# Performance work log

Measured on AMD Instinct MI355X. Metric: run time of the kernel, lower is better.

Reference implementation:

```python
import jax, jax.numpy as jnp
import numpy as np

N = 200000          # real (non-pad) faces
P = 8192            # pad entries
PAD = N + P         # padded table size
C_IN = 128
C_OUT = 128


def setup_inputs() -> dict:
    key = jax.random.key(0)
    ks = jax.random.split(key, 6)
    x = jax.random.normal(ks[0], (N, C_IN), jnp.float32)
    # column 0 = the face itself (a real, non-pad index); columns 1..8 = neighbors
    col0 = jnp.arange(N, dtype=jnp.int64)[:, None]
    nbrs = jax.random.randint(ks[1], (N, 8), 0, PAD, dtype=jnp.int64)
    face_neighborhood = jnp.concatenate([col0, nbrs], axis=1)
    face_is_pad = jnp.arange(PAD) >= N  # last P rows are padding
    s = 1.0 / np.sqrt(C_IN).astype(np.float32)
    in_proj_w = jax.random.normal(ks[2], (3 * C_IN, C_IN), jnp.float32) * s
    in_proj_b = jnp.zeros((3 * C_IN,), jnp.float32)
    out_proj_w = jax.random.normal(ks[3], (C_IN, C_IN), jnp.float32) * s
    out_proj_b = jnp.zeros((C_IN,), jnp.float32)
    conv_w = jax.random.normal(ks[4], (C_OUT, C_IN, 1, 2), jnp.float32) * (1.0 / np.sqrt(2.0 * C_IN).astype(np.float32))
    conv_b = jnp.zeros((C_OUT,), jnp.float32)
    return {
        "x": x,
        "face_neighborhood": face_neighborhood,
        "face_is_pad": face_is_pad,
        "pad_size": PAD,
        "in_proj_w": in_proj_w,
        "in_proj_b": in_proj_b,
        "out_proj_w": out_proj_w,
        "out_proj_b": out_proj_b,
        "conv_w": conv_w,
        "conv_b": conv_b,
    }


def reference(x, face_neighborhood, face_is_pad, pad_size,
              in_proj_w, in_proj_b, out_proj_w, out_proj_b, conv_w, conv_b):
    C = x.shape[1]
    H = max(1, C // 32)
    Dh = C // H
    # scatter real features into the padded table (padded_x[~face_is_pad] = x)
    nonpad_idx = jnp.nonzero(~face_is_pad, size=x.shape[0])[0]
    padded_x = jnp.zeros((pad_size, C), x.dtype).at[nonpad_idx].set(x)
    f = padded_x[face_neighborhood]              # [N, 9, C] 9-way gather
    center = f[:, 0]                             # [N, C] query feature
    kv = f[:, 1:]                                # [N, 8, C]
    # torch MultiheadAttention: packed in_proj then per-head scaled dot-product
    q = (center @ in_proj_w[:C].T + in_proj_b[:C]).reshape(-1, 1, H, Dh).transpose(0, 2, 1, 3)       # [N,H,1,Dh]
    k = (kv @ in_proj_w[C:2 * C].T + in_proj_b[C:2 * C]).reshape(-1, 8, H, Dh).transpose(0, 2, 1, 3)  # [N,H,8,Dh]
    v = (kv @ in_proj_w[2 * C:].T + in_proj_b[2 * C:]).reshape(-1, 8, H, Dh).transpose(0, 2, 1, 3)    # [N,H,8,Dh]
    scale = 1.0 / jnp.sqrt(jnp.asarray(Dh, q.dtype))
    scores = jnp.einsum('nhqd,nhkd->nhqk', q, k) * scale  # [N,H,1,8]
    pad_mask = face_is_pad[face_neighborhood[:, 1:]][:, None, None, :]  # [N,1,1,8]
    scores = jnp.where(pad_mask, -jnp.inf, scores)
    attn = jax.nn.softmax(scores, axis=-1)
    o = jnp.einsum('nhqk,nhkd->nhqd', attn, v)            # [N,H,1,Dh]
    o = o.transpose(0, 2, 1, 3).reshape(-1, C)            # [N,C] (q_len==1)
    h = o @ out_proj_w.T + out_proj_b                     # [N,C]
    # Conv2d(C_in, C_out, (1,2)) over [N, C, 1, 2] == linear fuse of center & h
    out = center @ conv_w[:, :, 0, 0].T + h @ conv_w[:, :, 0, 1].T + conv_b  # [N, C_out]
    return out
```

## Files before the change

kernel.cpp:

```cpp
#include <hip/hip_runtime.h>

typedef __bf16 bfrag __attribute__((ext_vector_type(8)));
typedef float f32x4 __attribute__((ext_vector_type(4)));

__device__ __forceinline__ unsigned short f2bf(float f) {
  unsigned u = __float_as_uint(f);
  u = (u + 0x7fffu + ((u >> 16) & 1u)) >> 16;
  return (unsigned short)u;
}
__device__ __forceinline__ float bflo(unsigned u) {
  return __uint_as_float(u << 16);
}
__device__ __forceinline__ float bfhi(unsigned u) {
  return __uint_as_float(u & 0xffff0000u);
}

#define LDA 136
#define LDB 72
#define LDT 136
#define LDK 72

__global__ void k_prep(const float* __restrict__ in_proj_w,
                       const float* __restrict__ conv_w,
                       const float* __restrict__ out_proj_w,
                       const float* __restrict__ out_proj_b,
                       const float* __restrict__ conv_b,
                       unsigned short* __restrict__ Wcat,
                       unsigned short* __restrict__ W2cat,
                       float* __restrict__ cvec) {
  int b = blockIdx.x, t = threadIdx.x;
  if (b < 384) {
    Wcat[b * 128 + t] = f2bf(in_proj_w[b * 128 + t]);
  } else {
    int c = b - 384;
    float s = 0.f;
    for (int k = 0; k < 128; ++k)
      s += conv_w[(c * 128 + k) * 2 + 1] * out_proj_w[k * 128 + t];
    W2cat[c * 256 + t] = f2bf(s);
    W2cat[c * 256 + 128 + t] = f2bf(conv_w[(c * 128 + t) * 2]);
    if (t == 0) {
      float cs = conv_b[c];
      for (int k = 0; k < 128; ++k)
        cs += conv_w[(c * 128 + k) * 2 + 1] * out_proj_b[k];
      cvec[c] = cs;
    }
  }
}

__global__ __launch_bounds__(256) void k_gemm_qkv(
    const float* __restrict__ x, const unsigned short* __restrict__ Wcat,
    const float* __restrict__ in_proj_b, unsigned short* __restrict__ Qb,
    unsigned short* __restrict__ KVb, int M) {
  __shared__ unsigned short sa[128 * LDA];
  __shared__ unsigned short sb[128 * LDB];
  const int m0 = blockIdx.x * 128;
  const int t = threadIdx.x;
  const int w = t >> 6, lane = t & 63, quad = lane >> 4, mr = lane & 15;

#pragma unroll
  for (int i = 0; i < 16; ++i) {
    int ch = t + 256 * i;
    int row = ch >> 5, col4 = ch & 31;
    float4 v = make_float4(0.f, 0.f, 0.f, 0.f);
    if (m0 + row < M)
      v = *reinterpret_cast<const float4*>(&x[(size_t)(m0 + row) * 128 + col4 * 4]);
    union { unsigned short s[4]; uint2 u; } p;
    p.s[0] = f2bf(v.x); p.s[1] = f2bf(v.y); p.s[2] = f2bf(v.z); p.s[3] = f2bf(v.w);
    *reinterpret_cast<uint2*>(&sa[row * LDA + col4 * 4]) = p.u;
  }
  __syncthreads();
  bfrag af[4][2];
#pragma unroll
  for (int ks = 0; ks < 4; ++ks) {
    int k0 = ks * 32 + quad * 8;
    af[ks][0] = *reinterpret_cast<const bfrag*>(&sa[(w * 32 + mr) * LDA + k0]);
    af[ks][1] = *reinterpret_cast<const bfrag*>(&sa[(w * 32 + 16 + mr) * LDA + k0]);
  }

#pragma unroll
  for (int cb = 0; cb < 3; ++cb) {
    f32x4 acc[2][8];
#pragma unroll
    for (int r = 0; r < 2; ++r)
#pragma unroll
      for (int c = 0; c < 8; ++c) acc[r][c] = (f32x4){0.f, 0.f, 0.f, 0.f};

#pragma unroll
    for (int kh = 0; kh < 2; ++kh) {
      __syncthreads();
#pragma unroll
      for (int i = 0; i < 4; ++i) {
        int ch = t + 256 * i;
        int row = ch >> 3, col8 = ch & 7;
        uint4 v = *reinterpret_cast<const uint4*>(
            &Wcat[(size_t)(cb * 128 + row) * 128 + kh * 64 + col8 * 8]);
        *reinterpret_cast<uint4*>(&sb[row * LDB + col8 * 8]) = v;
      }
      __syncthreads();
#pragma unroll
      for (int ks2 = 0; ks2 < 2; ++ks2) {
        int ks = kh * 2 + ks2;
        int k0 = ks2 * 32 + quad * 8;
#pragma unroll
        for (int c = 0; c < 8; ++c) {
          bfrag b = *reinterpret_cast<const bfrag*>(&sb[(c * 16 + mr) * LDB + k0]);
          acc[0][c] = __builtin_amdgcn_mfma_f32_16x16x32_bf16(af[ks][0], b, acc[0][c], 0, 0, 0);
          acc[1][c] = __builtin_amdgcn_mfma_f32_16x16x32_bf16(af[ks][1], b, acc[1][c], 0, 0, 0);
        }
      }
    }
    const float* bias = in_proj_b + cb * 128;
    __syncthreads();
#pragma unroll
    for (int r = 0; r < 2; ++r)
#pragma unroll
      for (int c = 0; c < 8; ++c) {
        int col = c * 16 + mr;
        float bv = bias[col];
#pragma unroll
        for (int g = 0; g < 4; ++g) {
          int row = w * 32 + r * 16 + quad * 4 + g;
          sa[row * LDT + col] = f2bf(acc[r][c][g] + bv);
        }
      }
    __syncthreads();
    unsigned short* dst = (cb == 0) ? Qb : KVb;
    const int ldst = (cb == 0) ? 128 : 256;
    const int cb_off = (cb == 2) ? 128 : 0;
#pragma unroll
    for (int i = 0; i < 8; ++i) {
      int ch = t + 256 * i;
      int row = ch >> 4, col8 = ch & 15;
      if (m0 + row < M) {
        uint4 v = *reinterpret_cast<const uint4*>(&sa[row * LDT + col8 * 8]);
        *reinterpret_cast<uint4*>(&dst[(size_t)(m0 + row) * ldst + cb_off + col8 * 8]) = v;
      }
    }
  }
}

__global__ __launch_bounds__(256) void k_attn(
    const unsigned short* __restrict__ Qb, const unsigned short* __restrict__ KVb,
    const int* __restrict__ fn, unsigned short* __restrict__ Ob, int M) {
  int w = threadIdx.x >> 6, lane = threadIdx.x & 63;
  int n = blockIdx.x * 4 + w;
  if (n >= M) return;
  const float scale = 0.17677669529663687f;
  const int l5 = lane & 31;
  uint2 qp = *reinterpret_cast<const uint2*>(&Qb[(size_t)n * 128 + 4 * l5]);
  float q0 = bflo(qp.x), q1 = bfhi(qp.x), q2 = bflo(qp.y), q3 = bfhi(qp.y);
  int idx[8];
#pragma unroll
  for (int j = 0; j < 8; ++j) idx[j] = fn[n * 9 + 1 + j];
  float o0 = 0.f, o1 = 0.f, o2 = 0.f, o3 = 0.f, sum = 0.f;
#pragma unroll
  for (int j = 0; j < 8; ++j) {
    bool valid = idx[j] < M;
    int id = valid ? idx[j] : 0;
    uint2 kv = *reinterpret_cast<const uint2*>(&KVb[(size_t)id * 256 + 4 * lane]);
    float a0 = bflo(kv.x), a1 = bfhi(kv.x), a2 = bflo(kv.y), a3 = bfhi(kv.y);
    float p = q0 * a0 + q1 * a1 + q2 * a2 + q3 * a3;
    p += __shfl_xor(p, 1);
    p += __shfl_xor(p, 2);
    p += __shfl_xor(p, 4);
    float pu = __shfl_xor(p, 32);
    float sf = (lane >= 32) ? pu : p;
    float s = valid ? sf * scale : -1e30f;
    float e = __expf(s);
    sum += e;
    o0 += e * a0; o1 += e * a1; o2 += e * a2; o3 += e * a3;
  }
  float inv = 1.f / sum;
  if (lane >= 32) {
    union { unsigned short s[4]; uint2 u; } p;
    p.s[0] = f2bf(o0 * inv); p.s[1] = f2bf(o1 * inv);
    p.s[2] = f2bf(o2 * inv); p.s[3] = f2bf(o3 * inv);
    *reinterpret_cast<uint2*>(&Ob[(size_t)n * 128 + 4 * l5]) = p.u;
  }
}

__global__ __launch_bounds__(256) void k_gemm_out(
    const unsigned short* __restrict__ Ob, const float* __restrict__ x,
    const unsigned short* __restrict__ W2cat, const float* __restrict__ cvec,
    float* __restrict__ out, int M) {
  __shared__ unsigned short sa[128 * LDK];
  __shared__ unsigned short sb[128 * LDK];
  const int m0 = blockIdx.x * 128;
  const int t = threadIdx.x;
  const int w = t >> 6, lane = t & 63, quad = lane >> 4, mr = lane & 15;

  f32x4 acc[2][8];
#pragma unroll
  for (int r = 0; r < 2; ++r)
#pragma unroll
    for (int c = 0; c < 8; ++c) acc[r][c] = (f32x4){0.f, 0.f, 0.f, 0.f};

  for (int kc = 0; kc < 4; ++kc) {
    if (kc < 2) {
#pragma unroll
      for (int i = 0; i < 4; ++i) {
        int ch = t + 256 * i;
        int row = ch >> 3, col8 = ch & 7;
        uint4 v = {0u, 0u, 0u, 0u};
        if (m0 + row < M)
          v = *reinterpret_cast<const uint4*>(&Ob[(size_t)(m0 + row) * 128 + kc * 64 + col8 * 8]);
        *reinterpret_cast<uint4*>(&sa[row * LDK + col8 * 8]) = v;
      }
    } else {
#pragma unroll
      for (int i = 0; i < 8; ++i) {
        int ch = t + 256 * i;
        int row = ch >> 4, col4 = ch & 15;
        float4 v = make_float4(0.f, 0.f, 0.f, 0.f);
        if (m0 + row < M)
          v = *reinterpret_cast<const float4*>(&x[(size_t)(m0 + row) * 128 + (kc - 2) * 64 + col4 * 4]);
        union { unsigned short s[4]; uint2 u; } p;
        p.s[0] = f2bf(v.x); p.s[1] = f2bf(v.y); p.s[2] = f2bf(v.z); p.s[3] = f2bf(v.w);
        *reinterpret_cast<uint2*>(&sa[row * LDK + col4 * 4]) = p.u;
      }
    }
#pragma unroll
    for (int i = 0; i < 4; ++i) {
      int ch = t + 256 * i;
      int row = ch >> 3, col8 = ch & 7;
      uint4 v = *reinterpret_cast<const uint4*>(&W2cat[(size_t)row * 256 + kc * 64 + col8 * 8]);
      *reinterpret_cast<uint4*>(&sb[row * LDK + col8 * 8]) = v;
    }
    __syncthreads();
#pragma unroll
    for (int ks = 0; ks < 2; ++ks) {
      int k0 = ks * 32 + quad * 8;
      bfrag a0 = *reinterpret_cast<const bfrag*>(&sa[(w * 32 + mr) * LDK + k0]);
      bfrag a1 = *reinterpret_cast<const bfrag*>(&sa[(w * 32 + 16 + mr) * LDK + k0]);
#pragma unroll
      for (int c = 0; c < 8; ++c) {
        bfrag b = *reinterpret_cast<const bfrag*>(&sb[(c * 16 + mr) * LDK + k0]);
        acc[0][c] = __builtin_amdgcn_mfma_f32_16x16x32_bf16(a0, b, acc[0][c], 0, 0, 0);
        acc[1][c] = __builtin_amdgcn_mfma_f32_16x16x32_bf16(a1, b, acc[1][c], 0, 0, 0);
      }
    }
    __syncthreads();
  }
#pragma unroll
  for (int r = 0; r < 2; ++r) {
    int rowbase = m0 + w * 32 + r * 16 + quad * 4;
#pragma unroll
    for (int c = 0; c < 8; ++c) {
      int col = c * 16 + mr;
      float cv = cvec[col];
#pragma unroll
      for (int g = 0; g < 4; ++g) {
        int row = rowbase + g;
        if (row < M) out[(size_t)row * 128 + col] = acc[r][c][g] + cv;
      }
    }
  }
}

extern "C" void kernel_launch(void* const* d_in, const int* in_sizes, int n_in,
                              void* d_out, int out_size, void* d_ws, size_t ws_size,
                              hipStream_t stream) {
  const float* x          = (const float*)d_in[0];
  const int*   fn         = (const int*)d_in[1];
  const float* in_proj_w  = (const float*)d_in[4];
  const float* in_proj_b  = (const float*)d_in[5];
  const float* out_proj_w = (const float*)d_in[6];
  const float* out_proj_b = (const float*)d_in[7];
  const float* conv_w     = (const float*)d_in[8];
  const float* conv_b     = (const float*)d_in[9];
  const int M = in_sizes[0] / 128;

  unsigned short* KVb = (unsigned short*)d_out;
  char* ws = (char*)d_ws;
  unsigned short* Qb    = (unsigned short*)ws;
  unsigned short* Ob    = (unsigned short*)(ws + (size_t)M * 128 * 2);
  unsigned short* Wcat  = (unsigned short*)(ws + (size_t)M * 128 * 4);
  unsigned short* W2cat = Wcat + 384 * 128;
  float*          cvec  = (float*)(W2cat + 128 * 256);

  const int mt = (M + 127) / 128;
  k_prep<<<dim3(512), dim3(128), 0, stream>>>(in_proj_w, conv_w, out_proj_w,
                                              out_proj_b, conv_b, Wcat, W2cat, cvec);
  k_gemm_qkv<<<dim3(mt), dim3(256), 0, stream>>>(x, Wcat, in_proj_b, Qb, KVb, M);
  k_attn<<<dim3((M + 3) / 4), dim3(256), 0, stream>>>(Qb, KVb, fn, Ob, M);
  k_gemm_out<<<dim3(mt), dim3(256), 0, stream>>>(Ob, x, W2cat, cvec, (float*)d_out, M);
}
```

Baseline: 471.8 us.

## Load GEMM A-fragments directly from global and stage epilogues through smaller LDS tiles

```diff
diff --git a/kernel.cpp b/kernel.cpp
--- a/kernel.cpp
+++ b/kernel.cpp
@@ -15,10 +15,9 @@
   return __uint_as_float(u & 0xffff0000u);
 }
 
-#define LDA 136
 #define LDB 72
-#define LDT 136
-#define LDK 72
+#define LDE 76
+#define LDO 36
 
 __global__ void k_prep(const float* __restrict__ in_proj_w,
                        const float* __restrict__ conv_w,
@@ -51,31 +50,31 @@
     const float* __restrict__ x, const unsigned short* __restrict__ Wcat,
     const float* __restrict__ in_proj_b, unsigned short* __restrict__ Qb,
     unsigned short* __restrict__ KVb, int M) {
-  __shared__ unsigned short sa[128 * LDA];
   __shared__ unsigned short sb[128 * LDB];
+  __shared__ unsigned short se[128 * LDE];
   const int m0 = blockIdx.x * 128;
   const int t = threadIdx.x;
   const int w = t >> 6, lane = t & 63, quad = lane >> 4, mr = lane & 15;
 
-#pragma unroll
-  for (int i = 0; i < 16; ++i) {
-    int ch = t + 256 * i;
-    int row = ch >> 5, col4 = ch & 31;
-    float4 v = make_float4(0.f, 0.f, 0.f, 0.f);
-    if (m0 + row < M)
-      v = *reinterpret_cast<const float4*>(&x[(size_t)(m0 + row) * 128 + col4 * 4]);
-    union { unsigned short s[4]; uint2 u; } p;
-    p.s[0] = f2bf(v.x); p.s[1] = f2bf(v.y); p.s[2] = f2bf(v.z); p.s[3] = f2bf(v.w);
-    *reinterpret_cast<uint2*>(&sa[row * LDA + col4 * 4]) = p.u;
-  }
-  __syncthreads();
   bfrag af[4][2];
 #pragma unroll
-  for (int ks = 0; ks < 4; ++ks) {
-    int k0 = ks * 32 + quad * 8;
-    af[ks][0] = *reinterpret_cast<const bfrag*>(&sa[(w * 32 + mr) * LDA + k0]);
-    af[ks][1] = *reinterpret_cast<const bfrag*>(&sa[(w * 32 + 16 + mr) * LDA + k0]);
-  }
+  for (int ks = 0; ks < 4; ++ks)
+#pragma unroll
+    for (int r = 0; r < 2; ++r) {
+      int row = m0 + w * 32 + r * 16 + mr;
+      union { unsigned short s[8]; bfrag f; } u;
+      if (row < M) {
+        const float4* p =
+            reinterpret_cast<const float4*>(&x[(size_t)row * 128 + ks * 32 + quad * 8]);
+        float4 v0 = p[0], v1 = p[1];
+        u.s[0] = f2bf(v0.x); u.s[1] = f2bf(v0.y); u.s[2] = f2bf(v0.z); u.s[3] = f2bf(v0.w);
+        u.s[4] = f2bf(v1.x); u.s[5] = f2bf(v1.y); u.s[6] = f2bf(v1.z); u.s[7] = f2bf(v1.w);
+      } else {
+#pragma unroll
+        for (int i = 0; i < 8; ++i) u.s[i] = 0;
+      }
+      af[ks][r] = u.f;
+    }
 
 #pragma unroll
   for (int cb = 0; cb < 3; ++cb) {
@@ -110,30 +109,36 @@
       }
     }
     const float* bias = in_proj_b + cb * 128;
-    __syncthreads();
-#pragma unroll
-    for (int r = 0; r < 2; ++r)
-#pragma unroll
-      for (int c = 0; c < 8; ++c) {
-        int col = c * 16 + mr;
-        float bv = bias[col];
-#pragma unroll
-        for (int g = 0; g < 4; ++g) {
-          int row = w * 32 + r * 16 + quad * 4 + g;
-          sa[row * LDT + col] = f2bf(acc[r][c][g] + bv);
-        }
-      }
-    __syncthreads();
     unsigned short* dst = (cb == 0) ? Qb : KVb;
     const int ldst = (cb == 0) ? 128 : 256;
     const int cb_off = (cb == 2) ? 128 : 0;
 #pragma unroll
-    for (int i = 0; i < 8; ++i) {
-      int ch = t + 256 * i;
-      int row = ch >> 4, col8 = ch & 15;
-      if (m0 + row < M) {
-        uint4 v = *reinterpret_cast<const uint4*>(&sa[row * LDT + col8 * 8]);
-        *reinterpret_cast<uint4*>(&dst[(size_t)(m0 + row) * ldst + cb_off + col8 * 8]) = v;
+    for (int p = 0; p < 2; ++p) {
+      __syncthreads();
+#pragma unroll
+      for (int r = 0; r < 2; ++r)
+#pragma unroll
+        for (int cc = 0; cc < 4; ++cc) {
+          int c = p * 4 + cc;
+          float bv = bias[c * 16 + mr];
+#pragma unroll
+          for (int g = 0; g < 4; ++g) {
+            int row = w * 32 + r * 16 + quad * 4 + g;
+            se[row * LDE + cc * 16 + mr] = f2bf(acc[r][c][g] + bv);
+          }
+        }
+      __syncthreads();
+#pragma unroll
+      for (int i = 0; i < 4; ++i) {
+        int ch = t + 256 * i;
+        int row = ch >> 3, col8 = ch & 7;
+        if (m0 + row < M) {
+          uint2 lo = *reinterpret_cast<const uint2*>(&se[row * LDE + col8 * 8]);
+          uint2 hi = *reinterpret_cast<const uint2*>(&se[row * LDE + col8 * 8 + 4]);
+          uint4 v = {lo.x, lo.y, hi.x, hi.y};
+          *reinterpret_cast<uint4*>(
+              &dst[(size_t)(m0 + row) * ldst + cb_off + p * 64 + col8 * 8]) = v;
+        }
       }
     }
   }
@@ -183,8 +188,8 @@
     const unsigned short* __restrict__ Ob, const float* __restrict__ x,
     const unsigned short* __restrict__ W2cat, const float* __restrict__ cvec,
     float* __restrict__ out, int M) {
-  __shared__ unsigned short sa[128 * LDK];
-  __shared__ unsigned short sb[128 * LDK];
+  __shared__ unsigned short sb[128 * LDB];
+  __shared__ float sf[128 * LDO];
   const int m0 = blockIdx.x * 128;
   const int t = threadIdx.x;
   const int w = t >> 6, lane = t & 63, quad = lane >> 4, mr = lane & 15;
@@ -195,63 +200,79 @@
 #pragma unroll
     for (int c = 0; c < 8; ++c) acc[r][c] = (f32x4){0.f, 0.f, 0.f, 0.f};
 
+#pragma unroll
   for (int kc = 0; kc < 4; ++kc) {
-    if (kc < 2) {
-#pragma unroll
-      for (int i = 0; i < 4; ++i) {
-        int ch = t + 256 * i;
-        int row = ch >> 3, col8 = ch & 7;
-        uint4 v = {0u, 0u, 0u, 0u};
-        if (m0 + row < M)
-          v = *reinterpret_cast<const uint4*>(&Ob[(size_t)(m0 + row) * 128 + kc * 64 + col8 * 8]);
-        *reinterpret_cast<uint4*>(&sa[row * LDK + col8 * 8]) = v;
-      }
-    } else {
-#pragma unroll
-      for (int i = 0; i < 8; ++i) {
-        int ch = t + 256 * i;
-        int row = ch >> 4, col4 = ch & 15;
-        float4 v = make_float4(0.f, 0.f, 0.f, 0.f);
-        if (m0 + row < M)
-          v = *reinterpret_cast<const float4*>(&x[(size_t)(m0 + row) * 128 + (kc - 2) * 64 + col4 * 4]);
-        union { unsigned short s[4]; uint2 u; } p;
-        p.s[0] = f2bf(v.x); p.s[1] = f2bf(v.y); p.s[2] = f2bf(v.z); p.s[3] = f2bf(v.w);
-        *reinterpret_cast<uint2*>(&sa[row * LDK + col4 * 4]) = p.u;
-      }
-    }
+    bfrag af[2][2];
+#pragma unroll
+    for (int ks2 = 0; ks2 < 2; ++ks2)
+#pragma unroll
+      for (int r = 0; r < 2; ++r) {
+        int row = m0 + w * 32 + r * 16 + mr;
+        if (kc < 2) {
+          union { uint4 v; bfrag f; } u;
+          u.v = make_uint4(0u, 0u, 0u, 0u);
+          if (row < M)
+            u.v = *reinterpret_cast<const uint4*>(
+                &Ob[(size_t)row * 128 + kc * 64 + ks2 * 32 + quad * 8]);
+          af[ks2][r] = u.f;
+        } else {
+          union { unsigned short s[8]; bfrag f; } u;
+          if (row < M) {
+            const float4* p = reinterpret_cast<const float4*>(
+                &x[(size_t)row * 128 + (kc - 2) * 64 + ks2 * 32 + quad * 8]);
+            float4 v0 = p[0], v1 = p[1];
+            u.s[0] = f2bf(v0.x); u.s[1] = f2bf(v0.y); u.s[2] = f2bf(v0.z); u.s[3] = f2bf(v0.w);
+            u.s[4] = f2bf(v1.x); u.s[5] = f2bf(v1.y); u.s[6] = f2bf(v1.z); u.s[7] = f2bf(v1.w);
+          } else {
+#pragma unroll
+            for (int i = 0; i < 8; ++i) u.s[i] = 0;
+          }
+          af[ks2][r] = u.f;
+        }
+      }
+    __syncthreads();
 #pragma unroll
     for (int i = 0; i < 4; ++i) {
       int ch = t + 256 * i;
       int row = ch >> 3, col8 = ch & 7;
       uint4 v = *reinterpret_cast<const uint4*>(&W2cat[(size_t)row * 256 + kc * 64 + col8 * 8]);
-      *reinterpret_cast<uint4*>(&sb[row * LDK + col8 * 8]) = v;
+      *reinterpret_cast<uint4*>(&sb[row * LDB + col8 * 8]) = v;
     }
     __syncthreads();
 #pragma unroll
-    for (int ks = 0; ks < 2; ++ks) {
-      int k0 = ks * 32 + quad * 8;
-      bfrag a0 = *reinterpret_cast<const bfrag*>(&sa[(w * 32 + mr) * LDK + k0]);
-      bfrag a1 = *reinterpret_cast<const bfrag*>(&sa[(w * 32 + 16 + mr) * LDK + k0]);
+    for (int ks2 = 0; ks2 < 2; ++ks2) {
+      int k0 = ks2 * 32 + quad * 8;
 #pragma unroll
       for (int c = 0; c < 8; ++c) {
-        bfrag b = *reinterpret_cast<const bfrag*>(&sb[(c * 16 + mr) * LDK + k0]);
-        acc[0][c] = __builtin_amdgcn_mfma_f32_16x16x32_bf16(a0, b, acc[0][c], 0, 0, 0);
-        acc[1][c] = __builtin_amdgcn_mfma_f32_16x16x32_bf16(a1, b, acc[1][c], 0, 0, 0);
-      }
-    }
+        bfrag b = *reinterpret_cast<const bfrag*>(&sb[(c * 16 + mr) * LDB + k0]);
+        acc[0][c] = __builtin_amdgcn_mfma_f32_16x16x32_bf16(af[ks2][0], b, acc[0][c], 0, 0, 0);
+        acc[1][c] = __builtin_amdgcn_mfma_f32_16x16x32_bf16(af[ks2][1], b, acc[1][c], 0, 0, 0);
+      }
+    }
+  }
+#pragma unroll
+  for (int p = 0; p < 4; ++p) {
     __syncthreads();
-  }
-#pragma unroll
-  for (int r = 0; r < 2; ++r) {
-    int rowbase = m0 + w * 32 + r * 16 + quad * 4;
-#pragma unroll
-    for (int c = 0; c < 8; ++c) {
-      int col = c * 16 + mr;
-      float cv = cvec[col];
-#pragma unroll
-      for (int g = 0; g < 4; ++g) {
-        int row = rowbase + g;
-        if (row < M) out[(size_t)row * 128 + col] = acc[r][c][g] + cv;
+#pragma unroll
+    for (int r = 0; r < 2; ++r)
+#pragma unroll
+      for (int cc = 0; cc < 2; ++cc) {
+        int c = p * 2 + cc;
+        float cv = cvec[c * 16 + mr];
+#pragma unroll
+        for (int g = 0; g < 4; ++g) {
+          int row = w * 32 + r * 16 + quad * 4 + g;
+          sf[row * LDO + cc * 16 + mr] = acc[r][c][g] + cv;
+        }
+      }
+    __syncthreads();
+#pragma unroll
+    for (int i = 0; i < 4; ++i) {
+      int ch = t + 256 * i;
+      int row = ch >> 3, col4 = ch & 7;
+      if (m0 + row < M) {
+        float4 v = *reinterpret_cast<const float4*>(&sf[row * LDO + col4 * 4]);
+        *reinterpret_cast<float4*>(&out[(size_t)(m0 + row) * 128 + p * 32 + col4 * 4]) = v;
       }
     }
   }
```

Measured after the change: 455.5 us. 3.5% less time.
